# Optimization experiments

Measured on AMD Instinct MI355X. Metric: run time of the kernel, lower is better.

The kernel has to match this reference:

```python
import jax, jax.numpy as jnp
import numpy as np

B, L, D_MODEL = 2, 1024, 1024
N_LAYERS = 2
D_INNER = 2 * D_MODEL          # expand = 2
D_STATE = 16
D_CONV = 4
DT_RANK = (D_MODEL + 15) // 16  # ceil(d_model/16) = 64
INIT_SCALE = 0.02


def setup_inputs() -> dict:
    key = jax.random.key(0)
    ks = jax.random.split(key, 8)
    f32 = jnp.float32
    dt_init = float(np.log(np.expm1(0.01)))  # softplus^-1(0.01), standard mamba dt bias init
    return {
        "x": jax.random.normal(ks[0], (B, L, D_MODEL), f32),
        "W_in": jax.random.normal(ks[1], (N_LAYERS, 2 * D_INNER, D_MODEL), f32) * INIT_SCALE,
        "conv_w": jax.random.normal(ks[2], (N_LAYERS, D_INNER, D_CONV), f32) * INIT_SCALE,
        "conv_b": jnp.zeros((N_LAYERS, D_INNER), f32),
        "W_x": jax.random.normal(ks[3], (N_LAYERS, DT_RANK + 2 * D_STATE, D_INNER), f32) * INIT_SCALE,
        "W_dt": jax.random.normal(ks[4], (N_LAYERS, D_INNER, DT_RANK), f32) * INIT_SCALE,
        "b_dt": jnp.full((N_LAYERS, D_INNER), dt_init, f32),
        "A_log": jnp.tile(jnp.log(jnp.arange(1, D_STATE + 1, dtype=f32)), (N_LAYERS, D_INNER, 1)),
        "D": jnp.ones((N_LAYERS, D_INNER), f32),
        "W_out": jax.random.normal(ks[5], (N_LAYERS, D_MODEL, D_INNER), f32) * INIT_SCALE,
    }


def _silu(x):
    return x * jax.nn.sigmoid(x)


def _causal_conv1d(u, w, b):
    # u: [B, L, D_INNER], w: [D_INNER, D_CONV] depthwise, b: [D_INNER]
    ut = jnp.pad(jnp.transpose(u, (0, 2, 1)), ((0, 0), (0, 0), (D_CONV - 1, 0)))
    y = jax.lax.conv_general_dilated(
        ut, w[:, None, :], window_strides=(1,), padding='VALID',
        feature_group_count=D_INNER, dimension_numbers=('NCH', 'OIH', 'NCH'))
    return jnp.transpose(y + b[None, :, None], (0, 2, 1))


def _selective_scan(u, dt, A, Bm, Cm, Dvec):
    # u, dt: [B, L, D_INNER]; A: [D_INNER, N]; Bm, Cm: [B, L, N]; Dvec: [D_INNER]
    dA = jnp.exp(dt[..., None] * A)                        # [B,L,Din,N]
    dBu = dt[..., None] * Bm[:, :, None, :] * u[..., None]  # [B,L,Din,N]

    def step(h, xs):
        dA_t, dBu_t, C_t = xs                              # [B,Din,N],[B,Din,N],[B,N]
        h = dA_t * h + dBu_t
        y = jnp.einsum('bdn,bn->bd', h, C_t)
        return h, y

    h0 = jnp.zeros((u.shape[0], D_INNER, D_STATE), u.dtype)
    _, ys = jax.lax.scan(step, h0, (jnp.swapaxes(dA, 0, 1),
                                    jnp.swapaxes(dBu, 0, 1),
                                    jnp.swapaxes(Cm, 0, 1)))
    return jnp.swapaxes(ys, 0, 1) + u * Dvec               # [B,L,Din]


def _mamba_layer(x, W_in, conv_w, conv_b, W_x, W_dt, b_dt, A_log, Dvec, W_out):
    xz = jnp.einsum('bld,ed->ble', x, W_in)                # [B,L,2*Din]
    u, z = jnp.split(xz, 2, axis=-1)
    u = _silu(_causal_conv1d(u, conv_w, conv_b))
    x_dbl = jnp.einsum('bld,rd->blr', u, W_x)              # [B,L,dt_rank+2N]
    dt, Bm, Cm = jnp.split(x_dbl, [DT_RANK, DT_RANK + D_STATE], axis=-1)
    dt = jax.nn.softplus(jnp.einsum('blr,dr->bld', dt, W_dt) + b_dt)
    A = -jnp.exp(A_log)
    y = _selective_scan(u, dt, A, Bm, Cm, Dvec)
    y = y * _silu(z)
    return jnp.einsum('bld,od->blo', y, W_out)


def reference(x, W_in, conv_w, conv_b, W_x, W_dt, b_dt, A_log, D, W_out):
    residual = x
    h = x
    for i in range(N_LAYERS):
        h = _mamba_layer(h, W_in[i], conv_w[i], conv_b[i], W_x[i],
                         W_dt[i], b_dt[i], A_log[i], D[i], W_out[i])
    return h + residual
```

## Files before the change

### kernel.cpp

```cpp
#include <hip/hip_runtime.h>
#include <hip/hip_bf16.h>
#include <math.h>

#define B_ 2
#define L_ 1024
#define DM 1024
#define DIN 2048
#define DS 16
#define DTR 64
#define CHL 32
#define NCH 32

typedef __attribute__((ext_vector_type(8))) short bf16x8;
typedef __attribute__((ext_vector_type(8))) unsigned short u16x8;
typedef __attribute__((ext_vector_type(4))) float f32x4;
typedef unsigned short ushort_t;
typedef unsigned int uint_t;

__device__ __forceinline__ float sigmoidf_(float x) { return 1.f / (1.f + __expf(-x)); }
__device__ __forceinline__ ushort_t f2b(float f) {
    uint_t b = __float_as_uint(f);
    return (ushort_t)((b + 0x7FFFu + ((b >> 16) & 1u)) >> 16);
}
__device__ __forceinline__ float b2f(ushort_t u) {
    return __uint_as_float(((uint_t)u) << 16);
}

__global__ __launch_bounds__(256) void f2b_all_k(
    const float* __restrict__ s0, ushort_t* __restrict__ d0, int n0,
    const float* __restrict__ s1, ushort_t* __restrict__ d1, int n1,
    const float* __restrict__ s2, ushort_t* __restrict__ d2, int n2,
    const float* __restrict__ s3, ushort_t* __restrict__ d3, int n3,
    const float* __restrict__ s4, ushort_t* __restrict__ d4, int n4)
{
    int i = blockIdx.x * 256 + threadIdx.x;
    if (i < n0) d0[i] = f2b(s0[i]);
    i -= n0;
    if (i >= 0 && i < n1) d1[i] = f2b(s1[i]);
    i -= n1;
    if (i >= 0 && i < n2) d2[i] = f2b(s2[i]);
    i -= n2;
    if (i >= 0 && i < n3) d3[i] = f2b(s3[i]);
    i -= n3;
    if (i >= 0 && i < n4) d4[i] = f2b(s4[i]);
}

__device__ __forceinline__ int xcd_swz(int wgid, int nwg) {
    int cpx = nwg >> 3;
    return (wgid & 7) * cpx + (wgid >> 3);
}

template<int EPI>
__global__ __launch_bounds__(256) void mgemm(const ushort_t* __restrict__ A,
    const ushort_t* __restrict__ Bt, float* __restrict__ Cf, ushort_t* __restrict__ Cb,
    const float* __restrict__ bias, int M, int N, int K, int lda, int ldb)
{
    __shared__ ushort_t sA[128 * 32];
    __shared__ ushort_t sB[128 * 32];
    const int tid = threadIdx.x;
    const int lane = tid & 63, wv = tid >> 6;
    const int wm = wv >> 1, wn = wv & 1;
    const int swz = xcd_swz(blockIdx.y * gridDim.x + blockIdx.x, gridDim.x * gridDim.y);
    const int m0 = (swz / gridDim.x) * 128, n0 = (swz % gridDim.x) * 128;
    const int sr = tid >> 2;
    const int sc = (tid & 3) * 8;
    f32x4 acc[4][4] = {};

    for (int k0 = 0; k0 < K; k0 += 32) {
#pragma unroll
        for (int j = 0; j < 2; ++j) {
            int ra = sr + j * 64;
            int ga = m0 + ra;
            __builtin_amdgcn_global_load_lds(
                (const uint_t*)(A + (size_t)ga * lda + k0 + sc),
                (uint_t*)(sA + ra * 32 + sc), 16, 0, 0);
            int gb = n0 + ra; if (gb >= N) gb = N - 1;
            __builtin_amdgcn_global_load_lds(
                (const uint_t*)(Bt + (size_t)gb * ldb + k0 + sc),
                (uint_t*)(sB + ra * 32 + sc), 16, 0, 0);
        }
        __syncthreads();
        bf16x8 af[4], bfr[4];
#pragma unroll
        for (int i = 0; i < 4; ++i) {
            af[i]  = *(const bf16x8*)(sA + (wm * 64 + i * 16 + (lane & 15)) * 32 + (lane >> 4) * 8);
            bfr[i] = *(const bf16x8*)(sB + (wn * 64 + i * 16 + (lane & 15)) * 32 + (lane >> 4) * 8);
        }
#pragma unroll
        for (int i = 0; i < 4; ++i)
#pragma unroll
            for (int jj = 0; jj < 4; ++jj)
                acc[i][jj] = __builtin_amdgcn_mfma_f32_16x16x32_bf16(af[i], bfr[jj], acc[i][jj], 0, 0, 0);
        __syncthreads();
    }

    const int cr = (lane >> 4) * 4, cc = lane & 15;
#pragma unroll
    for (int i = 0; i < 4; ++i) {
        int mrow = m0 + wm * 64 + i * 16 + cr;
#pragma unroll
        for (int jj = 0; jj < 4; ++jj) {
            int ncol = n0 + wn * 64 + jj * 16 + cc;
            if (ncol < N) {
#pragma unroll
                for (int r = 0; r < 4; ++r) {
                    float v = acc[i][jj][r];
                    size_t off = (size_t)(mrow + r) * N + ncol;
                    if (EPI == 2) {
                        float s = v + bias[ncol];
                        Cb[off] = f2b((s > 20.f) ? s : log1pf(expf(s)));
                    }
                    else { Cb[off] = f2b(v); }
                }
            }
        }
    }
    (void)Cf;
}

__global__ __launch_bounds__(256) void mgemm_sk(const ushort_t* __restrict__ A,
    const ushort_t* __restrict__ Bt, float* __restrict__ P,
    int M, int N, int Kslice, int lda, int ldb)
{
    __shared__ ushort_t sA[128 * 32];
    __shared__ ushort_t sB[128 * 32];
    const int tid = threadIdx.x;
    const int lane = tid & 63, wv = tid >> 6;
    const int wm = wv >> 1, wn = wv & 1;
    const int m0 = blockIdx.y * 128;
    const int kbase = blockIdx.z * Kslice;
    const int sr = tid >> 2;
    const int sc = (tid & 3) * 8;
    f32x4 acc[4][4] = {};

    for (int k0 = kbase; k0 < kbase + Kslice; k0 += 32) {
#pragma unroll
        for (int j = 0; j < 2; ++j) {
            int ra = sr + j * 64;
            __builtin_amdgcn_global_load_lds(
                (const uint_t*)(A + (size_t)(m0 + ra) * lda + k0 + sc),
                (uint_t*)(sA + ra * 32 + sc), 16, 0, 0);
            int gb = ra; if (gb >= N) gb = N - 1;
            __builtin_amdgcn_global_load_lds(
                (const uint_t*)(Bt + (size_t)gb * ldb + k0 + sc),
                (uint_t*)(sB + ra * 32 + sc), 16, 0, 0);
        }
        __syncthreads();
        bf16x8 af[4], bfr[4];
#pragma unroll
        for (int i = 0; i < 4; ++i) {
            af[i]  = *(const bf16x8*)(sA + (wm * 64 + i * 16 + (lane & 15)) * 32 + (lane >> 4) * 8);
            bfr[i] = *(const bf16x8*)(sB + (wn * 64 + i * 16 + (lane & 15)) * 32 + (lane >> 4) * 8);
        }
#pragma unroll
        for (int i = 0; i < 4; ++i)
#pragma unroll
            for (int jj = 0; jj < 4; ++jj)
                acc[i][jj] = __builtin_amdgcn_mfma_f32_16x16x32_bf16(af[i], bfr[jj], acc[i][jj], 0, 0, 0);
        __syncthreads();
    }

    const int cr = (lane >> 4) * 4, cc = lane & 15;
    float* Pz = P + (size_t)blockIdx.z * M * 96;
#pragma unroll
    for (int i = 0; i < 4; ++i) {
        int mrow = m0 + wm * 64 + i * 16 + cr;
#pragma unroll
        for (int jj = 0; jj < 4; ++jj) {
            int ncol = wn * 64 + jj * 16 + cc;
            if (ncol < 96) {
#pragma unroll
                for (int r = 0; r < 4; ++r)
                    Pz[(size_t)(mrow + r) * 96 + ncol] = acc[i][jj][r];
            }
        }
    }
}

__global__ __launch_bounds__(256) void wxred_k(const float* __restrict__ P,
    float* __restrict__ xdbl, ushort_t* __restrict__ xdblb)
{
    int idx = blockIdx.x * 256 + threadIdx.x;
    float s = 0.f;
#pragma unroll
    for (int z = 0; z < 8; ++z) s += P[(size_t)z * 196608 + idx];
    xdbl[idx] = s;
    xdblb[idx] = f2b(s);
}

template<int EPI>
__global__ __launch_bounds__(256) void mgemm_n64(const ushort_t* __restrict__ A,
    const ushort_t* __restrict__ Bt, float* __restrict__ Cf, ushort_t* __restrict__ Cb,
    const float* __restrict__ res, int M, int N, int K, int lda, int ldb)
{
    __shared__ ushort_t sA[128 * 32];
    __shared__ ushort_t sB[64 * 32];
    const int tid = threadIdx.x;
    const int lane = tid & 63, wv = tid >> 6;
    const int swz = xcd_swz(blockIdx.y * gridDim.x + blockIdx.x, gridDim.x * gridDim.y);
    const int m0 = (swz / gridDim.x) * 128, n0 = (swz % gridDim.x) * 64;
    const int sr = tid >> 2;
    const int sc = (tid & 3) * 8;
    f32x4 acc[2][4] = {};

    for (int k0 = 0; k0 < K; k0 += 32) {
#pragma unroll
        for (int j = 0; j < 2; ++j) {
            int ra = sr + j * 64;
            __builtin_amdgcn_global_load_lds(
                (const uint_t*)(A + (size_t)(m0 + ra) * lda + k0 + sc),
                (uint_t*)(sA + ra * 32 + sc), 16, 0, 0);
        }
        __builtin_amdgcn_global_load_lds(
            (const uint_t*)(Bt + (size_t)(n0 + sr) * ldb + k0 + sc),
            (uint_t*)(sB + sr * 32 + sc), 16, 0, 0);
        __syncthreads();
        bf16x8 af[2], bfr[4];
#pragma unroll
        for (int i = 0; i < 2; ++i)
            af[i]  = *(const bf16x8*)(sA + (wv * 32 + i * 16 + (lane & 15)) * 32 + (lane >> 4) * 8);
#pragma unroll
        for (int jj = 0; jj < 4; ++jj)
            bfr[jj] = *(const bf16x8*)(sB + (jj * 16 + (lane & 15)) * 32 + (lane >> 4) * 8);
#pragma unroll
        for (int i = 0; i < 2; ++i)
#pragma unroll
            for (int jj = 0; jj < 4; ++jj)
                acc[i][jj] = __builtin_amdgcn_mfma_f32_16x16x32_bf16(af[i], bfr[jj], acc[i][jj], 0, 0, 0);
        __syncthreads();
    }

    const int cr = (lane >> 4) * 4, cc = lane & 15;
#pragma unroll
    for (int i = 0; i < 2; ++i) {
        int mrow = m0 + wv * 32 + i * 16 + cr;
#pragma unroll
        for (int jj = 0; jj < 4; ++jj) {
            int ncol = n0 + jj * 16 + cc;
#pragma unroll
            for (int r = 0; r < 4; ++r) {
                float v = acc[i][jj][r];
                size_t off = (size_t)(mrow + r) * N + ncol;
                if (EPI == 3) Cb[off] = f2b(v);
                else Cf[off] = v + res[off];
            }
        }
    }
}

__global__ __launch_bounds__(256) void conv8_k(const ushort_t* __restrict__ xzb,
    const float* __restrict__ cw, const float* __restrict__ cb,
    ushort_t* __restrict__ ucb)
{
    int idx8 = blockIdx.x * 256 + threadIdx.x;
    int d8 = (idx8 & 255) * 8;
    int t = (idx8 >> 8) & (L_ - 1);
    int b = idx8 >> 18;
    const ushort_t* base = xzb + (size_t)b * L_ * (2 * DIN) + d8;
    float acc[8];
    const float4* cb4 = (const float4*)(cb + d8);
    float4 cbl = cb4[0], cbh = cb4[1];
#pragma unroll
    for (int e = 0; e < 4; ++e) { acc[e] = ((const float*)&cbl)[e]; acc[4 + e] = ((const float*)&cbh)[e]; }
    float4 cwv[8];
#pragma unroll
    for (int e = 0; e < 8; ++e) cwv[e] = ((const float4*)cw)[d8 + e];
#pragma unroll
    for (int j = 0; j < 4; ++j) {
        int tt = t - 3 + j;
        if (tt >= 0) {
            u16x8 row = *(const u16x8*)(base + (size_t)tt * (2 * DIN));
#pragma unroll
            for (int e = 0; e < 8; ++e)
                acc[e] = fmaf(((const float*)&cwv[e])[j], b2f(row[e]), acc[e]);
        }
    }
    u16x8 ob;
#pragma unroll
    for (int e = 0; e < 8; ++e) {
        float v = acc[e] * sigmoidf_(acc[e]);
        ob[e] = f2b(v);
    }
    *(u16x8*)(ucb + (size_t)idx8 * 8) = ob;
}

__global__ __launch_bounds__(256, 2) void scan_s1(const ushort_t* __restrict__ dtfb,
    const ushort_t* __restrict__ ucb, const float* __restrict__ xdbl,
    const float* __restrict__ A_log,
    float* __restrict__ bnd_q, float* __restrict__ bnd_s)
{
    __shared__ uint_t sdt[CHL * 256];
    __shared__ float sB[CHL * 16];
    const int tid = threadIdx.x;
    const int bx = blockIdx.x;
    const int dg = bx & 7, c = (bx >> 3) & 31, b = bx >> 8;
    const int d = dg * 256 + tid;
    const int row0 = b * L_ + c * CHL;

    float A_dn[16];
#pragma unroll
    for (int n = 0; n < 16; ++n) A_dn[n] = -__expf(A_log[(size_t)d * DS + n]);

    for (int k = 0; k < CHL; ++k) {
        size_t off = (size_t)(row0 + k) * DIN + d;
        sdt[k * 256 + tid] = (uint_t)dtfb[off] | ((uint_t)ucb[off] << 16);
    }
#pragma unroll
    for (int j = 0; j < 2; ++j) {
        int idx = tid + j * 256;
        int t = idx >> 4, n = idx & 15;
        sB[idx] = xdbl[(size_t)(row0 + t) * 96 + 64 + n];
    }
    __syncthreads();

    float q[16];
#pragma unroll
    for (int n = 0; n < 16; ++n) q[n] = 0.f;
    float s = 0.f;
    for (int k = 0; k < CHL; ++k) {
        uint_t pk = sdt[k * 256 + tid];
        float dtv = __uint_as_float(pk << 16);
        float uv  = __uint_as_float(pk & 0xffff0000u);
        float dtu = dtv * uv;
        s += dtv;
        f32x4 Bq[4];
#pragma unroll
        for (int j = 0; j < 4; ++j) Bq[j] = *(const f32x4*)(sB + k * 16 + j * 4);
#pragma unroll
        for (int n = 0; n < 16; ++n)
            q[n] = fmaf(__expf(dtv * A_dn[n]), q[n], dtu * Bq[n >> 2][n & 3]);
    }
    float* qp = bnd_q + ((size_t)(b * NCH + c) * DIN + d) * 16;
#pragma unroll
    for (int j = 0; j < 4; ++j)
        *(f32x4*)(qp + j * 4) = (f32x4){q[j * 4], q[j * 4 + 1], q[j * 4 + 2], q[j * 4 + 3]};
    bnd_s[(size_t)(b * NCH + c) * DIN + d] = s;
}

__global__ __launch_bounds__(256) void scan_b2(const float* __restrict__ bnd_q,
    const float* __restrict__ bnd_s, const float* __restrict__ A_log,
    float* __restrict__ Hini)
{
    int glob = blockIdx.x * 256 + threadIdx.x;
    int n = glob & 15, d = (glob >> 4) & (DIN - 1), b = glob >> 15;
    float A_dn = -__expf(A_log[(size_t)d * DS + n]);
    float H = 0.f;
    for (int c = 0; c < NCH; ++c) {
        size_t idx = (size_t)(b * NCH + c) * DIN + d;
        Hini[idx * 16 + n] = H;
        H = fmaf(__expf(A_dn * bnd_s[idx]), H, bnd_q[idx * 16 + n]);
    }
}

__global__ __launch_bounds__(256, 2) void scan_s2(const ushort_t* __restrict__ dtfb,
    const ushort_t* __restrict__ ucb_in, const float* __restrict__ xdbl,
    const ushort_t* __restrict__ xzb, const float* __restrict__ A_log,
    const float* __restrict__ Dvec, const float* __restrict__ Hini,
    ushort_t* __restrict__ ucb_out)
{
    __shared__ uint_t sdt[CHL * 256];
    __shared__ float sBC[CHL * 32];
    __shared__ float sy[CHL * 256];
    const int tid = threadIdx.x;
    const int bx = blockIdx.x;
    const int dg = bx & 7, c = (bx >> 3) & 31, b = bx >> 8;
    const int d = dg * 256 + tid;
    const int row0 = b * L_ + c * CHL;
    const float Dd = Dvec[d];

    float A_dn[16];
#pragma unroll
    for (int n = 0; n < 16; ++n) A_dn[n] = -__expf(A_log[(size_t)d * DS + n]);

    for (int k = 0; k < CHL; ++k) {
        size_t off = (size_t)(row0 + k) * DIN + d;
        sdt[k * 256 + tid] = (uint_t)dtfb[off] | ((uint_t)ucb_in[off] << 16);
    }
#pragma unroll
    for (int j = 0; j < 4; ++j) {
        int idx = tid + j * 256;
        int t = idx >> 5, jj = idx & 31;
        sBC[idx] = xdbl[(size_t)(row0 + t) * 96 + 64 + (jj & 1) * 16 + (jj >> 1)];
    }

    float h[16];
    const float* hp = Hini + ((size_t)(b * NCH + c) * DIN + d) * 16;
#pragma unroll
    for (int j = 0; j < 4; ++j) {
        f32x4 hv = *(const f32x4*)(hp + j * 4);
#pragma unroll
        for (int e = 0; e < 4; ++e) h[j * 4 + e] = hv[e];
    }
    __syncthreads();

    for (int k = 0; k < CHL; ++k) {
        uint_t pk = sdt[k * 256 + tid];
        float dtv = __uint_as_float(pk << 16);
        float uv  = __uint_as_float(pk & 0xffff0000u);
        float dtu = dtv * uv;
        float y = uv * Dd;
        f32x4 bcq[8];
#pragma unroll
        for (int j = 0; j < 8; ++j) bcq[j] = *(const f32x4*)(sBC + k * 32 + j * 4);
#pragma unroll
        for (int n = 0; n < 16; ++n) {
            float Bv = bcq[n >> 1][(n & 1) * 2];
            float Cv = bcq[n >> 1][(n & 1) * 2 + 1];
            h[n] = fmaf(__expf(dtv * A_dn[n]), h[n], dtu * Bv);
            y = fmaf(h[n], Cv, y);
        }
        sy[k * 256 + tid] = y;
    }
    __syncthreads();
    for (int k = 0; k < CHL; ++k) {
        float y = sy[k * 256 + tid];
        float z = b2f(xzb[(size_t)(row0 + k) * (2 * DIN) + DIN + d]);
        y *= z * sigmoidf_(z);
        ucb_out[(size_t)(row0 + k) * DIN + d] = f2b(y);
    }
}

extern "C" void kernel_launch(void* const* d_in, const int* in_sizes, int n_in,
                              void* d_out, int out_size, void* d_ws, size_t ws_size,
                              hipStream_t stream)
{
    (void)in_sizes; (void)n_in; (void)out_size; (void)ws_size;
    const float* x      = (const float*)d_in[0];
    const float* W_in   = (const float*)d_in[1];
    const float* conv_w = (const float*)d_in[2];
    const float* conv_b = (const float*)d_in[3];
    const float* W_x    = (const float*)d_in[4];
    const float* W_dt   = (const float*)d_in[5];
    const float* b_dt   = (const float*)d_in[6];
    const float* A_log  = (const float*)d_in[7];
    const float* Dv     = (const float*)d_in[8];
    const float* W_out  = (const float*)d_in[9];
    float* out = (float*)d_out;

    float* xdbl    = (float*)d_ws;
    float* pws     = xdbl + 196608;
    float* bnd_q   = pws + 1572864;
    float* bnd_s   = bnd_q + 2097152;
    float* Hini    = bnd_s + 131072;
    ushort_t* dtfb = (ushort_t*)(Hini + 2097152);
    ushort_t* xzb  = dtfb + 4194304;
    ushort_t* ucb  = xzb + 8388608;
    ushort_t* xdblb= ucb + 4194304;
    ushort_t* xb   = xdblb + 196608;
    ushort_t* wib  = xb + 2097152;
    ushort_t* wxb  = wib + 8388608;
    ushort_t* wdb  = wxb + 393216;
    ushort_t* wob  = wdb + 262144;

    const int M = B_ * L_;
    const int NT = 2097152 + 8388608 + 393216 + 262144 + 4194304;
    f2b_all_k<<<(NT + 255) / 256, 256, 0, stream>>>(
        x, xb, 2097152, W_in, wib, 8388608, W_x, wxb, 393216,
        W_dt, wdb, 262144, W_out, wob, 4194304);

    for (int layer = 0; layer < 2; ++layer) {
        mgemm<3><<<dim3(4096 / 128, M / 128), 256, 0, stream>>>(
            xb, wib + (size_t)layer * 4194304, nullptr, xzb, nullptr,
            M, 2 * DIN, DM, DM, DM);
        conv8_k<<<(B_ * L_ * DIN / 8) / 256, 256, 0, stream>>>(
            xzb, conv_w + (size_t)layer * DIN * 4, conv_b + (size_t)layer * DIN, ucb);
        mgemm_sk<<<dim3(1, M / 128, 8), 256, 0, stream>>>(
            ucb, wxb + (size_t)layer * 196608, pws, M, 96, DIN / 8, DIN, DIN);
        wxred_k<<<196608 / 256, 256, 0, stream>>>(pws, xdbl, xdblb);
        mgemm<2><<<dim3(2048 / 128, M / 128), 256, 0, stream>>>(
            xdblb, wdb + (size_t)layer * 131072, nullptr, dtfb,
            b_dt + (size_t)layer * DIN, M, DIN, DTR, 96, DTR);
        const float* Al = A_log + (size_t)layer * DIN * DS;
        scan_s1<<<B_ * NCH * 8, 256, 0, stream>>>(dtfb, ucb, xdbl, Al, bnd_q, bnd_s);
        scan_b2<<<(B_ * DIN * 16) / 256, 256, 0, stream>>>(bnd_q, bnd_s, Al, Hini);
        scan_s2<<<B_ * NCH * 8, 256, 0, stream>>>(dtfb, ucb, xdbl, xzb, Al,
            Dv + (size_t)layer * DIN, Hini, ucb);
        if (layer == 0)
            mgemm_n64<3><<<dim3(1024 / 64, M / 128), 256, 0, stream>>>(
                ucb, wob + (size_t)layer * 2097152, nullptr, xb, nullptr,
                M, DM, DIN, DIN, DIN);
        else
            mgemm_n64<4><<<dim3(1024 / 64, M / 128), 256, 0, stream>>>(
                ucb, wob + (size_t)layer * 2097152, out, nullptr, x,
                M, DM, DIN, DIN, DIN);
    }
}
```

Before: 479.4 us.

## Double-buffer GEMM LDS tiles, fold scan boundary pass into scan_s2, vectorize bf16 cast

```diff
diff --git a/kernel.cpp b/kernel.cpp
--- a/kernel.cpp
+++ b/kernel.cpp
@@ -13,6 +13,7 @@
 
 typedef __attribute__((ext_vector_type(8))) short bf16x8;
 typedef __attribute__((ext_vector_type(8))) unsigned short u16x8;
+typedef __attribute__((ext_vector_type(4))) unsigned short u16x4;
 typedef __attribute__((ext_vector_type(4))) float f32x4;
 typedef unsigned short ushort_t;
 typedef unsigned int uint_t;
@@ -33,16 +34,22 @@
     const float* __restrict__ s3, ushort_t* __restrict__ d3, int n3,
     const float* __restrict__ s4, ushort_t* __restrict__ d4, int n4)
 {
-    int i = blockIdx.x * 256 + threadIdx.x;
-    if (i < n0) d0[i] = f2b(s0[i]);
-    i -= n0;
-    if (i >= 0 && i < n1) d1[i] = f2b(s1[i]);
-    i -= n1;
-    if (i >= 0 && i < n2) d2[i] = f2b(s2[i]);
-    i -= n2;
-    if (i >= 0 && i < n3) d3[i] = f2b(s3[i]);
-    i -= n3;
-    if (i >= 0 && i < n4) d4[i] = f2b(s4[i]);
+    int i = (blockIdx.x * 256 + threadIdx.x) * 4;
+    const float* s; ushort_t* d;
+    if (i < n0) { s = s0; d = d0; }
+    else { i -= n0;
+    if (i < n1) { s = s1; d = d1; }
+    else { i -= n1;
+    if (i < n2) { s = s2; d = d2; }
+    else { i -= n2;
+    if (i < n3) { s = s3; d = d3; }
+    else { i -= n3;
+    if (i < n4) { s = s4; d = d4; }
+    else return; }}}}
+    float4 v = *(const float4*)(s + i);
+    u16x4 o;
+    o[0] = f2b(v.x); o[1] = f2b(v.y); o[2] = f2b(v.z); o[3] = f2b(v.w);
+    *(u16x4*)(d + i) = o;
 }
 
 __device__ __forceinline__ int xcd_swz(int wgid, int nwg) {
@@ -55,8 +62,8 @@
     const ushort_t* __restrict__ Bt, float* __restrict__ Cf, ushort_t* __restrict__ Cb,
     const float* __restrict__ bias, int M, int N, int K, int lda, int ldb)
 {
-    __shared__ ushort_t sA[128 * 32];
-    __shared__ ushort_t sB[128 * 32];
+    __shared__ ushort_t sA[2][128 * 32];
+    __shared__ ushort_t sB[2][128 * 32];
     const int tid = threadIdx.x;
     const int lane = tid & 63, wv = tid >> 6;
     const int wm = wv >> 1, wn = wv & 1;
@@ -66,25 +73,39 @@
     const int sc = (tid & 3) * 8;
     f32x4 acc[4][4] = {};
 
+#pragma unroll
+    for (int j = 0; j < 2; ++j) {
+        int ra = sr + j * 64;
+        __builtin_amdgcn_global_load_lds(
+            (const uint_t*)(A + (size_t)(m0 + ra) * lda + sc),
+            (uint_t*)(sA[0] + ra * 32 + sc), 16, 0, 0);
+        int gb = n0 + ra; if (gb >= N) gb = N - 1;
+        __builtin_amdgcn_global_load_lds(
+            (const uint_t*)(Bt + (size_t)gb * ldb + sc),
+            (uint_t*)(sB[0] + ra * 32 + sc), 16, 0, 0);
+    }
+    __syncthreads();
+    int cur = 0;
     for (int k0 = 0; k0 < K; k0 += 32) {
-#pragma unroll
-        for (int j = 0; j < 2; ++j) {
-            int ra = sr + j * 64;
-            int ga = m0 + ra;
-            __builtin_amdgcn_global_load_lds(
-                (const uint_t*)(A + (size_t)ga * lda + k0 + sc),
-                (uint_t*)(sA + ra * 32 + sc), 16, 0, 0);
-            int gb = n0 + ra; if (gb >= N) gb = N - 1;
-            __builtin_amdgcn_global_load_lds(
-                (const uint_t*)(Bt + (size_t)gb * ldb + k0 + sc),
-                (uint_t*)(sB + ra * 32 + sc), 16, 0, 0);
-        }
-        __syncthreads();
+        if (k0 + 32 < K) {
+            int nxt = cur ^ 1;
+#pragma unroll
+            for (int j = 0; j < 2; ++j) {
+                int ra = sr + j * 64;
+                __builtin_amdgcn_global_load_lds(
+                    (const uint_t*)(A + (size_t)(m0 + ra) * lda + k0 + 32 + sc),
+                    (uint_t*)(sA[nxt] + ra * 32 + sc), 16, 0, 0);
+                int gb = n0 + ra; if (gb >= N) gb = N - 1;
+                __builtin_amdgcn_global_load_lds(
+                    (const uint_t*)(Bt + (size_t)gb * ldb + k0 + 32 + sc),
+                    (uint_t*)(sB[nxt] + ra * 32 + sc), 16, 0, 0);
+            }
+        }
         bf16x8 af[4], bfr[4];
 #pragma unroll
         for (int i = 0; i < 4; ++i) {
-            af[i]  = *(const bf16x8*)(sA + (wm * 64 + i * 16 + (lane & 15)) * 32 + (lane >> 4) * 8);
-            bfr[i] = *(const bf16x8*)(sB + (wn * 64 + i * 16 + (lane & 15)) * 32 + (lane >> 4) * 8);
+            af[i]  = *(const bf16x8*)(sA[cur] + (wm * 64 + i * 16 + (lane & 15)) * 32 + (lane >> 4) * 8);
+            bfr[i] = *(const bf16x8*)(sB[cur] + (wn * 64 + i * 16 + (lane & 15)) * 32 + (lane >> 4) * 8);
         }
 #pragma unroll
         for (int i = 0; i < 4; ++i)
@@ -92,6 +113,7 @@
             for (int jj = 0; jj < 4; ++jj)
                 acc[i][jj] = __builtin_amdgcn_mfma_f32_16x16x32_bf16(af[i], bfr[jj], acc[i][jj], 0, 0, 0);
         __syncthreads();
+        cur ^= 1;
     }
 
     const int cr = (lane >> 4) * 4, cc = lane & 15;
@@ -122,8 +144,8 @@
     const ushort_t* __restrict__ Bt, float* __restrict__ P,
     int M, int N, int Kslice, int lda, int ldb)
 {
-    __shared__ ushort_t sA[128 * 32];
-    __shared__ ushort_t sB[128 * 32];
+    __shared__ ushort_t sA[2][128 * 32];
+    __shared__ ushort_t sB[2][128 * 32];
     const int tid = threadIdx.x;
     const int lane = tid & 63, wv = tid >> 6;
     const int wm = wv >> 1, wn = wv & 1;
@@ -133,24 +155,39 @@
     const int sc = (tid & 3) * 8;
     f32x4 acc[4][4] = {};
 
+#pragma unroll
+    for (int j = 0; j < 2; ++j) {
+        int ra = sr + j * 64;
+        __builtin_amdgcn_global_load_lds(
+            (const uint_t*)(A + (size_t)(m0 + ra) * lda + kbase + sc),
+            (uint_t*)(sA[0] + ra * 32 + sc), 16, 0, 0);
+        int gb = ra; if (gb >= N) gb = N - 1;
+        __builtin_amdgcn_global_load_lds(
+            (const uint_t*)(Bt + (size_t)gb * ldb + kbase + sc),
+            (uint_t*)(sB[0] + ra * 32 + sc), 16, 0, 0);
+    }
+    __syncthreads();
+    int cur = 0;
     for (int k0 = kbase; k0 < kbase + Kslice; k0 += 32) {
-#pragma unroll
-        for (int j = 0; j < 2; ++j) {
-            int ra = sr + j * 64;
-            __builtin_amdgcn_global_load_lds(
-                (const uint_t*)(A + (size_t)(m0 + ra) * lda + k0 + sc),
-                (uint_t*)(sA + ra * 32 + sc), 16, 0, 0);
-            int gb = ra; if (gb >= N) gb = N - 1;
-            __builtin_amdgcn_global_load_lds(
-                (const uint_t*)(Bt + (size_t)gb * ldb + k0 + sc),
-                (uint_t*)(sB + ra * 32 + sc), 16, 0, 0);
-        }
-        __syncthreads();
+        if (k0 + 32 < kbase + Kslice) {
+            int nxt = cur ^ 1;
+#pragma unroll
+            for (int j = 0; j < 2; ++j) {
+                int ra = sr + j * 64;
+                __builtin_amdgcn_global_load_lds(
+                    (const uint_t*)(A + (size_t)(m0 + ra) * lda + k0 + 32 + sc),
+                    (uint_t*)(sA[nxt] + ra * 32 + sc), 16, 0, 0);
+                int gb = ra; if (gb >= N) gb = N - 1;
+                __builtin_amdgcn_global_load_lds(
+                    (const uint_t*)(Bt + (size_t)gb * ldb + k0 + 32 + sc),
+                    (uint_t*)(sB[nxt] + ra * 32 + sc), 16, 0, 0);
+            }
+        }
         bf16x8 af[4], bfr[4];
 #pragma unroll
         for (int i = 0; i < 4; ++i) {
-            af[i]  = *(const bf16x8*)(sA + (wm * 64 + i * 16 + (lane & 15)) * 32 + (lane >> 4) * 8);
-            bfr[i] = *(const bf16x8*)(sB + (wn * 64 + i * 16 + (lane & 15)) * 32 + (lane >> 4) * 8);
+            af[i]  = *(const bf16x8*)(sA[cur] + (wm * 64 + i * 16 + (lane & 15)) * 32 + (lane >> 4) * 8);
+            bfr[i] = *(const bf16x8*)(sB[cur] + (wn * 64 + i * 16 + (lane & 15)) * 32 + (lane >> 4) * 8);
         }
 #pragma unroll
         for (int i = 0; i < 4; ++i)
@@ -158,6 +195,7 @@
             for (int jj = 0; jj < 4; ++jj)
                 acc[i][jj] = __builtin_amdgcn_mfma_f32_16x16x32_bf16(af[i], bfr[jj], acc[i][jj], 0, 0, 0);
         __syncthreads();
+        cur ^= 1;
     }
 
     const int cr = (lane >> 4) * 4, cc = lane & 15;
@@ -193,8 +231,8 @@
     const ushort_t* __restrict__ Bt, float* __restrict__ Cf, ushort_t* __restrict__ Cb,
     const float* __restrict__ res, int M, int N, int K, int lda, int ldb)
 {
-    __shared__ ushort_t sA[128 * 32];
-    __shared__ ushort_t sB[64 * 32];
+    __shared__ ushort_t sA[2][128 * 32];
+    __shared__ ushort_t sB[2][64 * 32];
     const int tid = threadIdx.x;
     const int lane = tid & 63, wv = tid >> 6;
     const int swz = xcd_swz(blockIdx.y * gridDim.x + blockIdx.x, gridDim.x * gridDim.y);
@@ -203,31 +241,46 @@
     const int sc = (tid & 3) * 8;
     f32x4 acc[2][4] = {};
 
+#pragma unroll
+    for (int j = 0; j < 2; ++j) {
+        int ra = sr + j * 64;
+        __builtin_amdgcn_global_load_lds(
+            (const uint_t*)(A + (size_t)(m0 + ra) * lda + sc),
+            (uint_t*)(sA[0] + ra * 32 + sc), 16, 0, 0);
+    }
+    __builtin_amdgcn_global_load_lds(
+        (const uint_t*)(Bt + (size_t)(n0 + sr) * ldb + sc),
+        (uint_t*)(sB[0] + sr * 32 + sc), 16, 0, 0);
+    __syncthreads();
+    int cur = 0;
     for (int k0 = 0; k0 < K; k0 += 32) {
-#pragma unroll
-        for (int j = 0; j < 2; ++j) {
-            int ra = sr + j * 64;
+        if (k0 + 32 < K) {
+            int nxt = cur ^ 1;
+#pragma unroll
+            for (int j = 0; j < 2; ++j) {
+                int ra = sr + j * 64;
+                __builtin_amdgcn_global_load_lds(
+                    (const uint_t*)(A + (size_t)(m0 + ra) * lda + k0 + 32 + sc),
+                    (uint_t*)(sA[nxt] + ra * 32 + sc), 16, 0, 0);
+            }
             __builtin_amdgcn_global_load_lds(
-                (const uint_t*)(A + (size_t)(m0 + ra) * lda + k0 + sc),
-                (uint_t*)(sA + ra * 32 + sc), 16, 0, 0);
-        }
-        __builtin_amdgcn_global_load_lds(
-            (const uint_t*)(Bt + (size_t)(n0 + sr) * ldb + k0 + sc),
-            (uint_t*)(sB + sr * 32 + sc), 16, 0, 0);
-        __syncthreads();
+                (const uint_t*)(Bt + (size_t)(n0 + sr) * ldb + k0 + 32 + sc),
+                (uint_t*)(sB[nxt] + sr * 32 + sc), 16, 0, 0);
+        }
         bf16x8 af[2], bfr[4];
 #pragma unroll
         for (int i = 0; i < 2; ++i)
-            af[i]  = *(const bf16x8*)(sA + (wv * 32 + i * 16 + (lane & 15)) * 32 + (lane >> 4) * 8);
+            af[i]  = *(const bf16x8*)(sA[cur] + (wv * 32 + i * 16 + (lane & 15)) * 32 + (lane >> 4) * 8);
 #pragma unroll
         for (int jj = 0; jj < 4; ++jj)
-            bfr[jj] = *(const bf16x8*)(sB + (jj * 16 + (lane & 15)) * 32 + (lane >> 4) * 8);
+            bfr[jj] = *(const bf16x8*)(sB[cur] + (jj * 16 + (lane & 15)) * 32 + (lane >> 4) * 8);
 #pragma unroll
         for (int i = 0; i < 2; ++i)
 #pragma unroll
             for (int jj = 0; jj < 4; ++jj)
                 acc[i][jj] = __builtin_amdgcn_mfma_f32_16x16x32_bf16(af[i], bfr[jj], acc[i][jj], 0, 0, 0);
         __syncthreads();
+        cur ^= 1;
     }
 
     const int cr = (lane >> 4) * 4, cc = lane & 15;
@@ -337,30 +390,14 @@
     bnd_s[(size_t)(b * NCH + c) * DIN + d] = s;
 }
 
-__global__ __launch_bounds__(256) void scan_b2(const float* __restrict__ bnd_q,
-    const float* __restrict__ bnd_s, const float* __restrict__ A_log,
-    float* __restrict__ Hini)
-{
-    int glob = blockIdx.x * 256 + threadIdx.x;
-    int n = glob & 15, d = (glob >> 4) & (DIN - 1), b = glob >> 15;
-    float A_dn = -__expf(A_log[(size_t)d * DS + n]);
-    float H = 0.f;
-    for (int c = 0; c < NCH; ++c) {
-        size_t idx = (size_t)(b * NCH + c) * DIN + d;
-        Hini[idx * 16 + n] = H;
-        H = fmaf(__expf(A_dn * bnd_s[idx]), H, bnd_q[idx * 16 + n]);
-    }
-}
-
 __global__ __launch_bounds__(256, 2) void scan_s2(const ushort_t* __restrict__ dtfb,
     const ushort_t* __restrict__ ucb_in, const float* __restrict__ xdbl,
     const ushort_t* __restrict__ xzb, const float* __restrict__ A_log,
-    const float* __restrict__ Dvec, const float* __restrict__ Hini,
-    ushort_t* __restrict__ ucb_out)
+    const float* __restrict__ Dvec, const float* __restrict__ bnd_q,
+    const float* __restrict__ bnd_s, ushort_t* __restrict__ ucb_out)
 {
     __shared__ uint_t sdt[CHL * 256];
     __shared__ float sBC[CHL * 32];
-    __shared__ float sy[CHL * 256];
     const int tid = threadIdx.x;
     const int bx = blockIdx.x;
     const int dg = bx & 7, c = (bx >> 3) & 31, b = bx >> 8;
@@ -384,12 +421,19 @@
     }
 
     float h[16];
-    const float* hp = Hini + ((size_t)(b * NCH + c) * DIN + d) * 16;
-#pragma unroll
-    for (int j = 0; j < 4; ++j) {
-        f32x4 hv = *(const f32x4*)(hp + j * 4);
-#pragma unroll
-        for (int e = 0; e < 4; ++e) h[j * 4 + e] = hv[e];
+#pragma unroll
+    for (int n = 0; n < 16; ++n) h[n] = 0.f;
+    const size_t cb_base = (size_t)b * NCH * DIN + d;
+    for (int cc = 0; cc < c; ++cc) {
+        size_t idx = cb_base + (size_t)cc * DIN;
+        float sv = bnd_s[idx];
+        const float* qp = bnd_q + idx * 16;
+        f32x4 qv[4];
+#pragma unroll
+        for (int j = 0; j < 4; ++j) qv[j] = *(const f32x4*)(qp + j * 4);
+#pragma unroll
+        for (int n = 0; n < 16; ++n)
+            h[n] = fmaf(__expf(A_dn[n] * sv), h[n], qv[n >> 2][n & 3]);
     }
     __syncthreads();
 
@@ -398,6 +442,7 @@
         float dtv = __uint_as_float(pk << 16);
         float uv  = __uint_as_float(pk & 0xffff0000u);
         float dtu = dtv * uv;
+        float z = b2f(xzb[(size_t)(row0 + k) * (2 * DIN) + DIN + d]);
         float y = uv * Dd;
         f32x4 bcq[8];
 #pragma unroll
@@ -409,12 +454,6 @@
             h[n] = fmaf(__expf(dtv * A_dn[n]), h[n], dtu * Bv);
             y = fmaf(h[n], Cv, y);
         }
-        sy[k * 256 + tid] = y;
-    }
-    __syncthreads();
-    for (int k = 0; k < CHL; ++k) {
-        float y = sy[k * 256 + tid];
-        float z = b2f(xzb[(size_t)(row0 + k) * (2 * DIN) + DIN + d]);
         y *= z * sigmoidf_(z);
         ucb_out[(size_t)(row0 + k) * DIN + d] = f2b(y);
     }
@@ -441,8 +480,7 @@
     float* pws     = xdbl + 196608;
     float* bnd_q   = pws + 1572864;
     float* bnd_s   = bnd_q + 2097152;
-    float* Hini    = bnd_s + 131072;
-    ushort_t* dtfb = (ushort_t*)(Hini + 2097152);
+    ushort_t* dtfb = (ushort_t*)(bnd_s + 131072);
     ushort_t* xzb  = dtfb + 4194304;
     ushort_t* ucb  = xzb + 8388608;
     ushort_t* xdblb= ucb + 4194304;
@@ -454,7 +492,7 @@
 
     const int M = B_ * L_;
     const int NT = 2097152 + 8388608 + 393216 + 262144 + 4194304;
-    f2b_all_k<<<(NT + 255) / 256, 256, 0, stream>>>(
+    f2b_all_k<<<(NT / 4) / 256, 256, 0, stream>>>(
         x, xb, 2097152, W_in, wib, 8388608, W_x, wxb, 393216,
         W_dt, wdb, 262144, W_out, wob, 4194304);
 
@@ -472,9 +510,8 @@
             b_dt + (size_t)layer * DIN, M, DIN, DTR, 96, DTR);
         const float* Al = A_log + (size_t)layer * DIN * DS;
         scan_s1<<<B_ * NCH * 8, 256, 0, stream>>>(dtfb, ucb, xdbl, Al, bnd_q, bnd_s);
-        scan_b2<<<(B_ * DIN * 16) / 256, 256, 0, stream>>>(bnd_q, bnd_s, Al, Hini);
         scan_s2<<<B_ * NCH * 8, 256, 0, stream>>>(dtfb, ucb, xdbl, xzb, Al,
-            Dv + (size_t)layer * DIN, Hini, ucb);
+            Dv + (size_t)layer * DIN, bnd_q, bnd_s, ucb);
         if (layer == 0)
             mgemm_n64<3><<<dim3(1024 / 64, M / 128), 256, 0, stream>>>(
                 ucb, wob + (size_t)layer * 2097152, nullptr, xb, nullptr,
```

Result: faster. 449.3 us (-6.3%).
